# Performance work log

Measured on AMD Instinct MI355X. Metric: run time of the kernel, lower is better.

The kernel has to match this reference:

```python
import jax, jax.numpy as jnp
import numpy as np

N, C, E = 2048, 512, 8192
EPS = 1e-5
MASK_FILL = -10000.0


def layer_norm(h, g, b):
    m = jnp.mean(h, axis=-1, keepdims=True)
    v = jnp.mean(jnp.square(h - m), axis=-1, keepdims=True)
    return (h - m) * jax.lax.rsqrt(v + EPS) * g + b


def setup_inputs() -> dict:
    key = jax.random.key(0)
    ks = jax.random.split(key, 20)
    s = 1.0 / np.sqrt(C)
    inp = {
        "x": jax.random.normal(ks[0], (N, C), jnp.float32),
        "edge_index": jax.random.randint(ks[1], (2, E), 0, N, jnp.int64),
        "edge_attr": jax.random.normal(ks[2], (E, C), jnp.float32),
        "edge_masks": jax.random.randint(ks[3], (E, E), 0, 2, jnp.int32).astype(bool),
        # GraphConv.nn: Linear(C, C)
        "W_nn": jax.random.normal(ks[4], (C, C), jnp.float32) * s,
        "b_nn": jax.random.normal(ks[5], (C,), jnp.float32) * s,
        # att_nn: Linear(3C, C) -> Tanh -> Linear(C, 1, bias=False) -> LeakyReLU(0.2)
        "W_att1": jax.random.normal(ks[6], (C, 3 * C), jnp.float32) * (1.0 / np.sqrt(3 * C)),
        "b_att1": jax.random.normal(ks[7], (C,), jnp.float32) * s,
        "w_att2": jax.random.normal(ks[8], (C,), jnp.float32) * s,
        # root weight [C, C] and bias [C]
        "root": jax.random.normal(ks[9], (C, C), jnp.float32) * s,
        "bias": jax.random.normal(ks[10], (C,), jnp.float32) * s,
        # graph_block: LayerNorms + Linear(C, C)
        "gamma1": jnp.ones((C,), jnp.float32),
        "beta1": jnp.zeros((C,), jnp.float32),
        "gamma2": jnp.ones((C,), jnp.float32),
        "beta2": jnp.zeros((C,), jnp.float32),
        "W_lin": jax.random.normal(ks[11], (C, C), jnp.float32) * s,
        "b_lin": jax.random.normal(ks[12], (C,), jnp.float32) * s,
    }
    return inp


def reference(x, edge_index, edge_attr, edge_masks, W_nn, b_nn, W_att1, b_att1,
              w_att2, root, bias, gamma1, beta1, gamma2, beta2, W_lin, b_lin):
    src = edge_index[0]  # x_j (source)
    dst = edge_index[1]  # x_i (target), also aggregation index

    # shared linear on gathered endpoints and edge attrs  [E, C]
    h_i = x[dst] @ W_nn.T + b_nn
    h_j = x[src] @ W_nn.T + b_nn
    h_e = edge_attr @ W_nn.T + b_nn

    # attention MLP (dropout in eval mode = identity)
    cat = jnp.concatenate([h_i, h_j, h_e], axis=1)          # [E, 3C]
    hid = jnp.tanh(cat @ W_att1.T + b_att1)                  # [E, C]
    s = hid @ w_att2                                         # [E]
    s = jax.nn.leaky_relu(s, 0.2)

    # row-wise masked softmax of the broadcast score vector; keep only diagonal
    logits = jnp.where(edge_masks, s[None, :], MASK_FILL)    # [E, E]
    lse = jax.scipy.special.logsumexp(logits, axis=1)        # [E]
    diag_logit = jnp.where(jnp.diagonal(edge_masks), s, MASK_FILL)
    att_diag = jnp.exp(diag_logit - lse)                     # [E]

    msg = h_j * att_diag[:, None]                            # [E, C]
    aggr = jax.ops.segment_sum(msg, dst, num_segments=N)     # [N, C]

    out = aggr + x @ root + bias                             # update()

    # graph_block wrapper
    x1 = layer_norm(out, gamma1, beta1)
    x2 = layer_norm(x1 + (x1 @ W_lin.T + b_lin), gamma2, beta2)
    return x2
```

## Files before the change

### kernel.cpp

```cpp
#include <hip/hip_runtime.h>
#include <hip/hip_bf16.h>
#include <stdint.h>
#include <stddef.h>

#define NN 2048
#define CD 512
#define EE 8192

typedef unsigned short u16;
typedef __attribute__((ext_vector_type(8))) short short8;
typedef __attribute__((ext_vector_type(4))) float floatx4;

__device__ inline u16 f2bf(float f) {
    uint32_t u = __float_as_uint(f);
    u += 0x7FFFu + ((u >> 16) & 1u);
    return (u16)(u >> 16);
}
__device__ inline float bf2f(u16 h) { return __uint_as_float(((uint32_t)h) << 16); }

__global__ __launch_bounds__(256) void prep_kernel(
    const float* __restrict__ x, const float* __restrict__ ea,
    const float* __restrict__ Wnn, const float* __restrict__ Wlin,
    const float* __restrict__ root, const float* __restrict__ Watt1,
    u16* __restrict__ xb, u16* __restrict__ eb, u16* __restrict__ Wnnb,
    u16* __restrict__ Wlinb, u16* __restrict__ rootTb, u16* __restrict__ Wpackb)
{
    size_t idx = (size_t)blockIdx.x * 256 + threadIdx.x;
    if (idx < 1048576) { xb[idx] = f2bf(x[idx]); return; }
    idx -= 1048576;
    if (idx < 4194304) { eb[idx] = f2bf(ea[idx]); return; }
    idx -= 4194304;
    if (idx < 262144) { Wnnb[idx] = f2bf(Wnn[idx]); return; }
    idx -= 262144;
    if (idx < 262144) { Wlinb[idx] = f2bf(Wlin[idx]); return; }
    idx -= 262144;
    if (idx < 262144) {
        int c = (int)(idx >> 9), k = (int)(idx & 511);
        rootTb[idx] = f2bf(root[(size_t)k * 512 + c]); return;
    }
    idx -= 262144;
    {
        int cp = (int)(idx >> 9), k = (int)(idx & 511);
        int s = cp >> 9, c = cp & 511;
        Wpackb[idx] = f2bf(Watt1[(size_t)c * 1536 + s * 512 + k]);
    }
}

template<int BM, int BN, bool OUT_BF16, bool BIAS>
__global__ __launch_bounds__(256) void gemm_bt(
    const u16* __restrict__ A, const u16* __restrict__ B,
    void* __restrict__ Cout, const float* __restrict__ bias, int Nc)
{
    constexpr int K = 512, BK = 32;
    __shared__ __align__(16) u16 As[BM * BK];
    __shared__ __align__(16) u16 Bs[BN * BK];
    const int tid = threadIdx.x;
    const int bm = blockIdx.x, bn = blockIdx.y;
    const int wave = tid >> 6, lane = tid & 63;
    const int wm = wave >> 1, wn = wave & 1;
    constexpr int WM = BM / 2, WN = BN / 2;
    constexpr int FM = WM / 16, FN = WN / 16;
    const int lrow = lane & 15, lk = lane >> 4;
    floatx4 acc[FM][FN] = {};
    constexpr int ALOADS = (BM * BK) / (256 * 8);
    constexpr int BLOADS = (BN * BK) / (256 * 8);

    for (int k0 = 0; k0 < K; k0 += BK) {
        __syncthreads();
#pragma unroll
        for (int c = 0; c < ALOADS; ++c) {
            int e = c * 2048 + tid * 8;
            int row = e >> 5, col = e & 31;
            __builtin_amdgcn_global_load_lds(
                (const __attribute__((address_space(1))) void*)(A + (size_t)(bm * BM + row) * K + k0 + col),
                (__attribute__((address_space(3))) void*)(&As[e]), 16, 0, 0);
        }
#pragma unroll
        for (int c = 0; c < BLOADS; ++c) {
            int e = c * 2048 + tid * 8;
            int row = e >> 5, col = e & 31;
            __builtin_amdgcn_global_load_lds(
                (const __attribute__((address_space(1))) void*)(B + (size_t)(bn * BN + row) * K + k0 + col),
                (__attribute__((address_space(3))) void*)(&Bs[e]), 16, 0, 0);
        }
        __syncthreads();

        short8 af[FM], bfr[FN];
#pragma unroll
        for (int i = 0; i < FM; ++i)
            af[i] = *(const short8*)(&As[(wm * WM + i * 16 + lrow) * BK + lk * 8]);
#pragma unroll
        for (int j = 0; j < FN; ++j)
            bfr[j] = *(const short8*)(&Bs[(wn * WN + j * 16 + lrow) * BK + lk * 8]);
#pragma unroll
        for (int i = 0; i < FM; ++i)
#pragma unroll
            for (int j = 0; j < FN; ++j)
                acc[i][j] = __builtin_amdgcn_mfma_f32_16x16x32_bf16(af[i], bfr[j], acc[i][j], 0, 0, 0);
    }

#pragma unroll
    for (int i = 0; i < FM; ++i) {
#pragma unroll
        for (int j = 0; j < FN; ++j) {
            const int col = bn * BN + wn * WN + j * 16 + lrow;
            const float bv = BIAS ? bias[col] : 0.0f;
#pragma unroll
            for (int r = 0; r < 4; ++r) {
                const int row = bm * BM + wm * WM + i * 16 + lk * 4 + r;
                const float v = acc[i][j][r] + bv;
                if (OUT_BF16) ((u16*)Cout)[(size_t)row * Nc + col] = f2bf(v);
                else          ((float*)Cout)[(size_t)row * Nc + col] = v;
            }
        }
    }
}

__global__ __launch_bounds__(256) void edge_score(
    const float* __restrict__ G12, const float* __restrict__ G3,
    const int* __restrict__ ei, const float* __restrict__ batt1,
    const float* __restrict__ watt2, float* __restrict__ sOut)
{
    const int e = blockIdx.x;
    const int src = ei[e];
    const int dst = ei[EE + e];
    const int tid = threadIdx.x;
    const float* g1 = G12 + (size_t)dst * 1024;
    const float* g2 = G12 + (size_t)src * 1024 + 512;
    const float* g3 = G3 + (size_t)e * 512;
    float partial = 0.0f;
#pragma unroll
    for (int c = tid; c < 512; c += 256) {
        float v = tanhf(g1[c] + g2[c] + g3[c] + batt1[c]);
        partial += v * watt2[c];
    }
    for (int o = 32; o; o >>= 1) partial += __shfl_down(partial, o);
    __shared__ float red[4];
    if ((tid & 63) == 0) red[tid >> 6] = partial;
    __syncthreads();
    if (tid == 0) {
        float sv = red[0] + red[1] + red[2] + red[3];
        sOut[e] = (sv >= 0.0f) ? sv : 0.2f * sv;
    }
}

__global__ __launch_bounds__(1024) void softmax_prep(
    const float* __restrict__ s, float* __restrict__ p)
{
    const int tid = threadIdx.x;
    float m = -3.0e38f;
    for (int j = tid; j < EE; j += 1024) m = fmaxf(m, s[j]);
    for (int o = 32; o; o >>= 1) m = fmaxf(m, __shfl_down(m, o));
    __shared__ float red[16];
    if ((tid & 63) == 0) red[tid >> 6] = m;
    __syncthreads();
    float M = red[0];
#pragma unroll
    for (int k = 1; k < 16; ++k) M = fmaxf(M, red[k]);
    for (int j = tid; j < EE; j += 1024) p[j] = __expf(s[j] - M);
}

__global__ __launch_bounds__(256) void lse_att(
    const unsigned char* __restrict__ mask, const float* __restrict__ p,
    float* __restrict__ att)
{
    const int i = blockIdx.x;
    const int tid = threadIdx.x;
    const unsigned char* row = mask + (size_t)i * EE;
    float sum = 0.0f;
#pragma unroll
    for (int c = 0; c < 2; ++c) {
        const int base = c * 4096 + tid * 16;
        uint4 mw = *(const uint4*)(row + base);
        uint32_t w[4] = { mw.x, mw.y, mw.z, mw.w };
#pragma unroll
        for (int q = 0; q < 4; ++q) {
            float4 pv = *(const float4*)(p + base + q * 4);
            uint32_t b = w[q];
            sum += pv.x * (float)(b & 1u);
            sum += pv.y * (float)((b >> 8) & 1u);
            sum += pv.z * (float)((b >> 16) & 1u);
            sum += pv.w * (float)((b >> 24) & 1u);
        }
    }
    for (int o = 32; o; o >>= 1) sum += __shfl_down(sum, o);
    __shared__ float red[4];
    if ((tid & 63) == 0) red[tid >> 6] = sum;
    __syncthreads();
    if (tid == 0) {
        float total = red[0] + red[1] + red[2] + red[3];
        unsigned char diag = mask[(size_t)i * EE + i];
        float a;
        if (total > 0.0f) a = diag ? (p[i] / total) : 0.0f;
        else              a = 1.0f / (float)EE;
        att[i] = a;
    }
}

__global__ __launch_bounds__(256) void aggr_kernel(
    const u16* __restrict__ Hb, const int* __restrict__ ei,
    const float* __restrict__ att, float* __restrict__ OUT1)
{
    const int e = blockIdx.x;
    const float a = att[e];
    if (a == 0.0f) return;
    const int src = ei[e];
    const int dst = ei[EE + e];
    const u16* h = Hb + (size_t)src * 512;
    float* o = OUT1 + (size_t)dst * 512;
    for (int c = threadIdx.x; c < 512; c += 256)
        atomicAdd(o + c, a * bf2f(h[c]));
}

template<bool RESID, bool WRITE_BF16>
__global__ __launch_bounds__(256) void ln_kernel(
    const float* __restrict__ in, const float* __restrict__ resid,
    const float* __restrict__ gamma, const float* __restrict__ beta,
    float* __restrict__ outF, u16* __restrict__ outB)
{
    const int n = blockIdx.x, tid = threadIdx.x;
    const size_t rowoff = (size_t)n * 512;
    float2 v = *(const float2*)(in + rowoff + tid * 2);
    float a0 = v.x, a1 = v.y;
    if (RESID) {
        float2 r = *(const float2*)(resid + rowoff + tid * 2);
        a0 += r.x; a1 += r.y;
    }
    float sum = a0 + a1, sq = a0 * a0 + a1 * a1;
    for (int o = 32; o; o >>= 1) {
        sum += __shfl_down(sum, o);
        sq  += __shfl_down(sq, o);
    }
    __shared__ float rs_[4], rq_[4];
    if ((tid & 63) == 0) { rs_[tid >> 6] = sum; rq_[tid >> 6] = sq; }
    __syncthreads();
    sum = rs_[0] + rs_[1] + rs_[2] + rs_[3];
    sq  = rq_[0] + rq_[1] + rq_[2] + rq_[3];
    const float mean = sum * (1.0f / 512.0f);
    const float var  = sq * (1.0f / 512.0f) - mean * mean;
    const float rstd = rsqrtf(var + 1e-5f);
    const int c0 = tid * 2;
    const float y0 = (a0 - mean) * rstd * gamma[c0]     + beta[c0];
    const float y1 = (a1 - mean) * rstd * gamma[c0 + 1] + beta[c0 + 1];
    *(float2*)(outF + rowoff + c0) = make_float2(y0, y1);
    if (WRITE_BF16) { outB[rowoff + c0] = f2bf(y0); outB[rowoff + c0 + 1] = f2bf(y1); }
}

extern "C" void kernel_launch(void* const* d_in, const int* in_sizes, int n_in,
                              void* d_out, int out_size, void* d_ws, size_t ws_size,
                              hipStream_t stream)
{
    const float* x     = (const float*)d_in[0];
    const int*   ei    = (const int*)d_in[1];
    const float* ea    = (const float*)d_in[2];
    const unsigned char* mask = (const unsigned char*)d_in[3];
    const float* Wnn   = (const float*)d_in[4];
    const float* bnn   = (const float*)d_in[5];
    const float* Watt1 = (const float*)d_in[6];
    const float* batt1 = (const float*)d_in[7];
    const float* watt2 = (const float*)d_in[8];
    const float* root  = (const float*)d_in[9];
    const float* bias  = (const float*)d_in[10];
    const float* gam1  = (const float*)d_in[11];
    const float* bet1  = (const float*)d_in[12];
    const float* gam2  = (const float*)d_in[13];
    const float* bet2  = (const float*)d_in[14];
    const float* Wlin  = (const float*)d_in[15];
    const float* blin  = (const float*)d_in[16];
    float* out = (float*)d_out;

    char* w = (char*)d_ws;
    auto take = [&](size_t bytes) -> char* {
        char* pp = w;
        w += (bytes + 255) & ~(size_t)255;
        return pp;
    };
    u16*   xb     = (u16*)take((size_t)NN * CD * 2);
    u16*   eb     = (u16*)take((size_t)EE * CD * 2);
    u16*   Wnnb   = (u16*)take((size_t)CD * CD * 2);
    u16*   Wlinb  = (u16*)take((size_t)CD * CD * 2);
    u16*   rootTb = (u16*)take((size_t)CD * CD * 2);
    u16*   Wpb    = (u16*)take((size_t)3 * CD * CD * 2);
    u16*   Hb     = (u16*)take((size_t)NN * CD * 2);
    u16*   HEb    = (u16*)take((size_t)EE * CD * 2);
    float* G12    = (float*)take((size_t)NN * 1024 * 4);
    float* G3     = (float*)take((size_t)EE * CD * 4);
    float* OUT1   = (float*)take((size_t)NN * CD * 4);
    float* sbuf   = (float*)take((size_t)EE * 4);
    float* pbuf   = (float*)take((size_t)EE * 4);
    float* attb   = (float*)take((size_t)EE * 4);
    float* x1     = (float*)take((size_t)NN * CD * 4);
    u16*   x1b    = (u16*)take((size_t)NN * CD * 2);
    float* Tbuf   = (float*)take((size_t)NN * CD * 4);

    prep_kernel<<<26624, 256, 0, stream>>>(x, ea, Wnn, Wlin, root, Watt1,
                                           xb, eb, Wnnb, Wlinb, rootTb, Wpb);
    gemm_bt<64, 128, true, true><<<dim3(32, 4), 256, 0, stream>>>(xb, Wnnb, Hb, bnn, 512);
    gemm_bt<128, 128, true, true><<<dim3(64, 4), 256, 0, stream>>>(eb, Wnnb, HEb, bnn, 512);
    gemm_bt<64, 128, false, false><<<dim3(32, 8), 256, 0, stream>>>(Hb, Wpb, G12, nullptr, 1024);
    gemm_bt<128, 128, false, false><<<dim3(64, 4), 256, 0, stream>>>(HEb, Wpb + (size_t)1024 * 512, G3, nullptr, 512);
    gemm_bt<64, 128, false, true><<<dim3(32, 4), 256, 0, stream>>>(xb, rootTb, OUT1, bias, 512);
    edge_score<<<EE, 256, 0, stream>>>(G12, G3, ei, batt1, watt2, sbuf);
    softmax_prep<<<1, 1024, 0, stream>>>(sbuf, pbuf);
    lse_att<<<EE, 256, 0, stream>>>(mask, pbuf, attb);
    aggr_kernel<<<EE, 256, 0, stream>>>(Hb, ei, attb, OUT1);
    ln_kernel<false, true><<<NN, 256, 0, stream>>>(OUT1, nullptr, gam1, bet1, x1, x1b);
    gemm_bt<64, 128, false, true><<<dim3(32, 4), 256, 0, stream>>>(x1b, Wlinb, Tbuf, blin, 512);
    ln_kernel<true, false><<<NN, 256, 0, stream>>>(Tbuf, x1, gam2, bet2, out, nullptr);
}
```

Baseline: 465.1 us.

## Precompose attention weights with Wnn and fuse edge GEMM with tanh score reduction

Folds W_nn into the attention weights by precomputing Watt1·Wnn products and a combined bias vector, so the node and edge paths each need one GEMM. The x-side GEMMs (h, root, G12) run as one concatenated-B node GEMM. The edge GEMM now applies tanh and dot with w_att2 in its epilogue and accumulates scores atomically, removing the HEb and G3 intermediates and the separate edge_score pass. Also vectorizes prep conversion, processes four mask rows per block in lse_att, and vectorizes aggr loads. This changes bf16 rounding order, since products are quantized after composition, and adds atomics plus a memset.

```diff
diff --git a/kernel.cpp b/kernel.cpp
--- a/kernel.cpp
+++ b/kernel.cpp
@@ -1,5 +1,4 @@
 #include <hip/hip_runtime.h>
-#include <hip/hip_bf16.h>
 #include <stdint.h>
 #include <stddef.h>
 
@@ -22,49 +21,79 @@
     const float* __restrict__ x, const float* __restrict__ ea,
     const float* __restrict__ Wnn, const float* __restrict__ Wlin,
     const float* __restrict__ root, const float* __restrict__ Watt1,
-    u16* __restrict__ xb, u16* __restrict__ eb, u16* __restrict__ Wnnb,
-    u16* __restrict__ Wlinb, u16* __restrict__ rootTb, u16* __restrict__ Wpackb)
-{
-    size_t idx = (size_t)blockIdx.x * 256 + threadIdx.x;
-    if (idx < 1048576) { xb[idx] = f2bf(x[idx]); return; }
-    idx -= 1048576;
-    if (idx < 4194304) { eb[idx] = f2bf(ea[idx]); return; }
-    idx -= 4194304;
-    if (idx < 262144) { Wnnb[idx] = f2bf(Wnn[idx]); return; }
-    idx -= 262144;
-    if (idx < 262144) { Wlinb[idx] = f2bf(Wlin[idx]); return; }
-    idx -= 262144;
-    if (idx < 262144) {
-        int c = (int)(idx >> 9), k = (int)(idx & 511);
-        rootTb[idx] = f2bf(root[(size_t)k * 512 + c]); return;
-    }
-    idx -= 262144;
+    u16* __restrict__ xb, u16* __restrict__ eb, u16* __restrict__ Bcat,
+    u16* __restrict__ WnnTb, u16* __restrict__ Wlinb, u16* __restrict__ Wpackb)
+{
+    size_t i4 = ((size_t)blockIdx.x * 256 + threadIdx.x) * 4;
+    auto cvt4 = [](const float* src, u16* dst, size_t idx) {
+        float4 v = *(const float4*)(src + idx);
+        ushort4 o; o.x = f2bf(v.x); o.y = f2bf(v.y); o.z = f2bf(v.z); o.w = f2bf(v.w);
+        *(ushort4*)(dst + idx) = o;
+    };
+    if (i4 < 1048576) { cvt4(x, xb, i4); return; }
+    i4 -= 1048576;
+    if (i4 < 4194304) { cvt4(ea, eb, i4); return; }
+    i4 -= 4194304;
+    if (i4 < 262144) { cvt4(Wnn, Bcat, i4); return; }
+    i4 -= 262144;
+    if (i4 < 262144) {
+        int c = (int)(i4 >> 9), k = (int)(i4 & 511);
+        ushort4 o;
+        o.x = f2bf(root[(size_t)(k + 0) * 512 + c]);
+        o.y = f2bf(root[(size_t)(k + 1) * 512 + c]);
+        o.z = f2bf(root[(size_t)(k + 2) * 512 + c]);
+        o.w = f2bf(root[(size_t)(k + 3) * 512 + c]);
+        *(ushort4*)(Bcat + 262144 + i4) = o; return;
+    }
+    i4 -= 262144;
+    if (i4 < 262144) {
+        int k = (int)(i4 >> 9), t = (int)(i4 & 511);
+        ushort4 o;
+        o.x = f2bf(Wnn[(size_t)(t + 0) * 512 + k]);
+        o.y = f2bf(Wnn[(size_t)(t + 1) * 512 + k]);
+        o.z = f2bf(Wnn[(size_t)(t + 2) * 512 + k]);
+        o.w = f2bf(Wnn[(size_t)(t + 3) * 512 + k]);
+        *(ushort4*)(WnnTb + i4) = o; return;
+    }
+    i4 -= 262144;
+    if (i4 < 262144) { cvt4(Wlin, Wlinb, i4); return; }
+    i4 -= 262144;
     {
-        int cp = (int)(idx >> 9), k = (int)(idx & 511);
-        int s = cp >> 9, c = cp & 511;
-        Wpackb[idx] = f2bf(Watt1[(size_t)c * 1536 + s * 512 + k]);
-    }
-}
-
-template<int BM, int BN, bool OUT_BF16, bool BIAS>
-__global__ __launch_bounds__(256) void gemm_bt(
-    const u16* __restrict__ A, const u16* __restrict__ B,
-    void* __restrict__ Cout, const float* __restrict__ bias, int Nc)
-{
-    constexpr int K = 512, BK = 32;
-    __shared__ __align__(16) u16 As[BM * BK];
-    __shared__ __align__(16) u16 Bs[BN * BK];
-    const int tid = threadIdx.x;
-    const int bm = blockIdx.x, bn = blockIdx.y;
+        int cp = (int)(i4 >> 9), t = (int)(i4 & 511);
+        const float* sp = Watt1 + (size_t)(cp & 511) * 1536 + (cp >> 9) * 512 + t;
+        float4 v = *(const float4*)sp;
+        ushort4 o; o.x = f2bf(v.x); o.y = f2bf(v.y); o.z = f2bf(v.z); o.w = f2bf(v.w);
+        *(ushort4*)(Wpackb + i4) = o;
+    }
+}
+
+__global__ __launch_bounds__(256) void bbvec_kernel(
+    const float* __restrict__ Watt1, const float* __restrict__ bnn,
+    const float* __restrict__ batt1, float* __restrict__ bb)
+{
+    const int c = blockIdx.x, tid = threadIdx.x;
+    const float* row = Watt1 + (size_t)c * 1536;
+    float partial = 0.0f;
+#pragma unroll
+    for (int t = tid; t < 1536; t += 256) partial += row[t] * bnn[t & 511];
+    for (int o = 32; o; o >>= 1) partial += __shfl_down(partial, o);
+    __shared__ float red[4];
+    if ((tid & 63) == 0) red[tid >> 6] = partial;
+    __syncthreads();
+    if (tid == 0) bb[c] = batt1[c] + red[0] + red[1] + red[2] + red[3];
+}
+
+template<int BM, int BN>
+__device__ inline void gemm_core(const u16* __restrict__ A, const u16* __restrict__ B,
+                                 int bm, int bn, int tid, u16* As, u16* Bs,
+                                 floatx4 (&acc)[BM / 32][BN / 32])
+{
+    constexpr int K = 512, BK = 32, WM = BM / 2, WN = BN / 2, FM = WM / 16, FN = WN / 16;
     const int wave = tid >> 6, lane = tid & 63;
     const int wm = wave >> 1, wn = wave & 1;
-    constexpr int WM = BM / 2, WN = BN / 2;
-    constexpr int FM = WM / 16, FN = WN / 16;
     const int lrow = lane & 15, lk = lane >> 4;
-    floatx4 acc[FM][FN] = {};
     constexpr int ALOADS = (BM * BK) / (256 * 8);
     constexpr int BLOADS = (BN * BK) / (256 * 8);
-
     for (int k0 = 0; k0 < K; k0 += BK) {
         __syncthreads();
 #pragma unroll
@@ -84,7 +113,6 @@
                 (__attribute__((address_space(3))) void*)(&Bs[e]), 16, 0, 0);
         }
         __syncthreads();
-
         short8 af[FM], bfr[FN];
 #pragma unroll
         for (int i = 0; i < FM; ++i)
@@ -98,9 +126,23 @@
             for (int j = 0; j < FN; ++j)
                 acc[i][j] = __builtin_amdgcn_mfma_f32_16x16x32_bf16(af[i], bfr[j], acc[i][j], 0, 0, 0);
     }
-
-#pragma unroll
-    for (int i = 0; i < FM; ++i) {
+}
+
+template<int BM, int BN, bool OUT_BF16, bool BIAS>
+__global__ __launch_bounds__(256) void gemm_bt(
+    const u16* __restrict__ A, const u16* __restrict__ B,
+    void* __restrict__ Cout, const float* __restrict__ bias, int Nc)
+{
+    __shared__ __align__(16) u16 As[BM * 32];
+    __shared__ __align__(16) u16 Bs[BN * 32];
+    constexpr int WM = BM / 2, WN = BN / 2, FM = WM / 16, FN = WN / 16;
+    floatx4 acc[FM][FN] = {};
+    const int tid = threadIdx.x, bm = blockIdx.x, bn = blockIdx.y;
+    gemm_core<BM, BN>(A, B, bm, bn, tid, As, Bs, acc);
+    const int wave = tid >> 6, lane = tid & 63, wm = wave >> 1, wn = wave & 1;
+    const int lrow = lane & 15, lk = lane >> 4;
+#pragma unroll
+    for (int i = 0; i < FM; ++i)
 #pragma unroll
         for (int j = 0; j < FN; ++j) {
             const int col = bn * BN + wn * WN + j * 16 + lrow;
@@ -113,43 +155,89 @@
                 else          ((float*)Cout)[(size_t)row * Nc + col] = v;
             }
         }
-    }
-}
-
-__global__ __launch_bounds__(256) void edge_score(
-    const float* __restrict__ G12, const float* __restrict__ G3,
-    const int* __restrict__ ei, const float* __restrict__ batt1,
-    const float* __restrict__ watt2, float* __restrict__ sOut)
-{
-    const int e = blockIdx.x;
-    const int src = ei[e];
-    const int dst = ei[EE + e];
+}
+
+__global__ __launch_bounds__(256) void node_gemm(
+    const u16* __restrict__ A, const u16* __restrict__ B,
+    const float* __restrict__ bnn, const float* __restrict__ bias,
+    u16* __restrict__ Hb, float* __restrict__ OUT1, float* __restrict__ G12)
+{
+    __shared__ __align__(16) u16 As[128 * 32];
+    __shared__ __align__(16) u16 Bs[128 * 32];
+    floatx4 acc[4][4] = {};
+    const int tid = threadIdx.x, bm = blockIdx.x, bn = blockIdx.y;
+    gemm_core<128, 128>(A, B, bm, bn, tid, As, Bs, acc);
+    const int wave = tid >> 6, lane = tid & 63, wm = wave >> 1, wn = wave & 1;
+    const int lrow = lane & 15, lk = lane >> 4;
+#pragma unroll
+    for (int i = 0; i < 4; ++i)
+#pragma unroll
+        for (int j = 0; j < 4; ++j) {
+            const int colg = bn * 128 + wn * 64 + j * 16 + lrow;
+#pragma unroll
+            for (int r = 0; r < 4; ++r) {
+                const int row = bm * 128 + wm * 64 + i * 16 + lk * 4 + r;
+                const float v = acc[i][j][r];
+                if (bn < 4) {
+                    Hb[(size_t)row * 512 + colg] = f2bf(v + bnn[colg]);
+                } else if (bn < 8) {
+                    const int c = colg - 512;
+                    OUT1[(size_t)row * 512 + c] = v + bias[c];
+                } else {
+                    G12[(size_t)row * 1024 + (colg - 1024)] = v;
+                }
+            }
+        }
+}
+
+__global__ __launch_bounds__(256) void edge_gemm_score(
+    const u16* __restrict__ A, const u16* __restrict__ B,
+    const float* __restrict__ G12, const int* __restrict__ ei,
+    const float* __restrict__ bb, const float* __restrict__ w2,
+    float* __restrict__ sraw)
+{
+    __shared__ __align__(16) u16 As[128 * 32];
+    __shared__ __align__(16) u16 Bs[128 * 32];
+    floatx4 acc[4][4] = {};
+    const int tid = threadIdx.x, bm = blockIdx.x, bn = blockIdx.y;
+    gemm_core<128, 128>(A, B, bm, bn, tid, As, Bs, acc);
+    const int wave = tid >> 6, lane = tid & 63, wm = wave >> 1, wn = wave & 1;
+    const int lrow = lane & 15, lk = lane >> 4;
+#pragma unroll
+    for (int i = 0; i < 4; ++i) {
+#pragma unroll
+        for (int r = 0; r < 4; ++r) {
+            const int e = bm * 128 + wm * 64 + i * 16 + lk * 4 + r;
+            const int sn = ei[e], dn = ei[EE + e];
+            float sp = 0.0f;
+#pragma unroll
+            for (int j = 0; j < 4; ++j) {
+                const int col = bn * 128 + wn * 64 + j * 16 + lrow;
+                const float v = acc[i][j][r]
+                              + G12[(size_t)dn * 1024 + col]
+                              + G12[(size_t)sn * 1024 + 512 + col]
+                              + bb[col];
+                sp += tanhf(v) * w2[col];
+            }
+#pragma unroll
+            for (int m = 1; m < 16; m <<= 1) sp += __shfl_xor(sp, m);
+            if (lrow == 0) atomicAdd(sraw + e, sp);
+        }
+    }
+}
+
+__global__ __launch_bounds__(1024) void softmax_prep(
+    const float* __restrict__ sraw, float* __restrict__ p)
+{
     const int tid = threadIdx.x;
-    const float* g1 = G12 + (size_t)dst * 1024;
-    const float* g2 = G12 + (size_t)src * 1024 + 512;
-    const float* g3 = G3 + (size_t)e * 512;
-    float partial = 0.0f;
-#pragma unroll
-    for (int c = tid; c < 512; c += 256) {
-        float v = tanhf(g1[c] + g2[c] + g3[c] + batt1[c]);
-        partial += v * watt2[c];
-    }
-    for (int o = 32; o; o >>= 1) partial += __shfl_down(partial, o);
-    __shared__ float red[4];
-    if ((tid & 63) == 0) red[tid >> 6] = partial;
-    __syncthreads();
-    if (tid == 0) {
-        float sv = red[0] + red[1] + red[2] + red[3];
-        sOut[e] = (sv >= 0.0f) ? sv : 0.2f * sv;
-    }
-}
-
-__global__ __launch_bounds__(1024) void softmax_prep(
-    const float* __restrict__ s, float* __restrict__ p)
-{
-    const int tid = threadIdx.x;
+    float sv[8];
     float m = -3.0e38f;
-    for (int j = tid; j < EE; j += 1024) m = fmaxf(m, s[j]);
+#pragma unroll
+    for (int k = 0; k < 8; ++k) {
+        float v = sraw[k * 1024 + tid];
+        v = (v >= 0.0f) ? v : 0.2f * v;
+        sv[k] = v; m = fmaxf(m, v);
+    }
     for (int o = 32; o; o >>= 1) m = fmaxf(m, __shfl_down(m, o));
     __shared__ float red[16];
     if ((tid & 63) == 0) red[tid >> 6] = m;
@@ -157,39 +245,51 @@
     float M = red[0];
 #pragma unroll
     for (int k = 1; k < 16; ++k) M = fmaxf(M, red[k]);
-    for (int j = tid; j < EE; j += 1024) p[j] = __expf(s[j] - M);
+#pragma unroll
+    for (int k = 0; k < 8; ++k) p[k * 1024 + tid] = __expf(sv[k] - M);
 }
 
 __global__ __launch_bounds__(256) void lse_att(
     const unsigned char* __restrict__ mask, const float* __restrict__ p,
     float* __restrict__ att)
 {
-    const int i = blockIdx.x;
-    const int tid = threadIdx.x;
-    const unsigned char* row = mask + (size_t)i * EE;
-    float sum = 0.0f;
+    const int i0 = blockIdx.x * 4, tid = threadIdx.x;
+    float sums[4] = {0.0f, 0.0f, 0.0f, 0.0f};
 #pragma unroll
     for (int c = 0; c < 2; ++c) {
         const int base = c * 4096 + tid * 16;
-        uint4 mw = *(const uint4*)(row + base);
-        uint32_t w[4] = { mw.x, mw.y, mw.z, mw.w };
-#pragma unroll
-        for (int q = 0; q < 4; ++q) {
-            float4 pv = *(const float4*)(p + base + q * 4);
-            uint32_t b = w[q];
-            sum += pv.x * (float)(b & 1u);
-            sum += pv.y * (float)((b >> 8) & 1u);
-            sum += pv.z * (float)((b >> 16) & 1u);
-            sum += pv.w * (float)((b >> 24) & 1u);
-        }
-    }
-    for (int o = 32; o; o >>= 1) sum += __shfl_down(sum, o);
-    __shared__ float red[4];
-    if ((tid & 63) == 0) red[tid >> 6] = sum;
+        float pv[16];
+#pragma unroll
+        for (int q = 0; q < 4; ++q)
+            *(float4*)(pv + q * 4) = *(const float4*)(p + base + q * 4);
+#pragma unroll
+        for (int rr = 0; rr < 4; ++rr) {
+            uint4 mw = *(const uint4*)(mask + (size_t)(i0 + rr) * EE + base);
+            uint32_t w[4] = { mw.x, mw.y, mw.z, mw.w };
+            float s = 0.0f;
+#pragma unroll
+            for (int q = 0; q < 4; ++q) {
+                s += pv[q * 4 + 0] * (float)((w[q]      ) & 1u);
+                s += pv[q * 4 + 1] * (float)((w[q] >>  8) & 1u);
+                s += pv[q * 4 + 2] * (float)((w[q] >> 16) & 1u);
+                s += pv[q * 4 + 3] * (float)((w[q] >> 24) & 1u);
+            }
+            sums[rr] += s;
+        }
+    }
+#pragma unroll
+    for (int rr = 0; rr < 4; ++rr)
+        for (int o = 32; o; o >>= 1) sums[rr] += __shfl_down(sums[rr], o);
+    __shared__ float red[4][4];
+    if ((tid & 63) == 0) {
+#pragma unroll
+        for (int rr = 0; rr < 4; ++rr) red[rr][tid >> 6] = sums[rr];
+    }
     __syncthreads();
-    if (tid == 0) {
-        float total = red[0] + red[1] + red[2] + red[3];
-        unsigned char diag = mask[(size_t)i * EE + i];
+    if (tid < 4) {
+        const int i = i0 + tid;
+        const float total = red[tid][0] + red[tid][1] + red[tid][2] + red[tid][3];
+        const unsigned char diag = mask[(size_t)i * EE + i];
         float a;
         if (total > 0.0f) a = diag ? (p[i] / total) : 0.0f;
         else              a = 1.0f / (float)EE;
@@ -204,12 +304,13 @@
     const int e = blockIdx.x;
     const float a = att[e];
     if (a == 0.0f) return;
-    const int src = ei[e];
-    const int dst = ei[EE + e];
-    const u16* h = Hb + (size_t)src * 512;
-    float* o = OUT1 + (size_t)dst * 512;
-    for (int c = threadIdx.x; c < 512; c += 256)
-        atomicAdd(o + c, a * bf2f(h[c]));
+    const int sn = ei[e], dn = ei[EE + e];
+    const u16* h = Hb + (size_t)sn * 512;
+    float* o = OUT1 + (size_t)dn * 512;
+    const int c = threadIdx.x * 2;
+    const uint32_t hv = *(const uint32_t*)(h + c);
+    atomicAdd(o + c,     a * bf2f((u16)(hv & 0xffffu)));
+    atomicAdd(o + c + 1, a * bf2f((u16)(hv >> 16)));
 }
 
 template<bool RESID, bool WRITE_BF16>
@@ -227,10 +328,7 @@
         a0 += r.x; a1 += r.y;
     }
     float sum = a0 + a1, sq = a0 * a0 + a1 * a1;
-    for (int o = 32; o; o >>= 1) {
-        sum += __shfl_down(sum, o);
-        sq  += __shfl_down(sq, o);
-    }
+    for (int o = 32; o; o >>= 1) { sum += __shfl_down(sum, o); sq += __shfl_down(sq, o); }
     __shared__ float rs_[4], rq_[4];
     if ((tid & 63) == 0) { rs_[tid >> 6] = sum; rq_[tid >> 6] = sq; }
     __syncthreads();
@@ -271,38 +369,36 @@
 
     char* w = (char*)d_ws;
     auto take = [&](size_t bytes) -> char* {
-        char* pp = w;
-        w += (bytes + 255) & ~(size_t)255;
-        return pp;
+        char* pp = w; w += (bytes + 255) & ~(size_t)255; return pp;
     };
     u16*   xb     = (u16*)take((size_t)NN * CD * 2);
     u16*   eb     = (u16*)take((size_t)EE * CD * 2);
-    u16*   Wnnb   = (u16*)take((size_t)CD * CD * 2);
+    u16*   Wpackb = (u16*)take((size_t)1536 * CD * 2);
+    u16*   WnnTb  = (u16*)take((size_t)CD * CD * 2);
     u16*   Wlinb  = (u16*)take((size_t)CD * CD * 2);
-    u16*   rootTb = (u16*)take((size_t)CD * CD * 2);
-    u16*   Wpb    = (u16*)take((size_t)3 * CD * CD * 2);
+    u16*   Bcat   = (u16*)take((size_t)2560 * CD * 2);
     u16*   Hb     = (u16*)take((size_t)NN * CD * 2);
-    u16*   HEb    = (u16*)take((size_t)EE * CD * 2);
     float* G12    = (float*)take((size_t)NN * 1024 * 4);
-    float* G3     = (float*)take((size_t)EE * CD * 4);
     float* OUT1   = (float*)take((size_t)NN * CD * 4);
-    float* sbuf   = (float*)take((size_t)EE * 4);
+    float* sraw   = (float*)take((size_t)EE * 4);
     float* pbuf   = (float*)take((size_t)EE * 4);
     float* attb   = (float*)take((size_t)EE * 4);
+    float* bb     = (float*)take((size_t)CD * 4);
     float* x1     = (float*)take((size_t)NN * CD * 4);
     u16*   x1b    = (u16*)take((size_t)NN * CD * 2);
     float* Tbuf   = (float*)take((size_t)NN * CD * 4);
 
-    prep_kernel<<<26624, 256, 0, stream>>>(x, ea, Wnn, Wlin, root, Watt1,
-                                           xb, eb, Wnnb, Wlinb, rootTb, Wpb);
-    gemm_bt<64, 128, true, true><<<dim3(32, 4), 256, 0, stream>>>(xb, Wnnb, Hb, bnn, 512);
-    gemm_bt<128, 128, true, true><<<dim3(64, 4), 256, 0, stream>>>(eb, Wnnb, HEb, bnn, 512);
-    gemm_bt<64, 128, false, false><<<dim3(32, 8), 256, 0, stream>>>(Hb, Wpb, G12, nullptr, 1024);
-    gemm_bt<128, 128, false, false><<<dim3(64, 4), 256, 0, stream>>>(HEb, Wpb + (size_t)1024 * 512, G3, nullptr, 512);
-    gemm_bt<64, 128, false, true><<<dim3(32, 4), 256, 0, stream>>>(xb, rootTb, OUT1, bias, 512);
-    edge_score<<<EE, 256, 0, stream>>>(G12, G3, ei, batt1, watt2, sbuf);
-    softmax_prep<<<1, 1024, 0, stream>>>(sbuf, pbuf);
-    lse_att<<<EE, 256, 0, stream>>>(mask, pbuf, attb);
+    hipMemsetAsync(sraw, 0, (size_t)EE * 4, stream);
+    prep_kernel<<<6912, 256, 0, stream>>>(x, ea, Wnn, Wlin, root, Watt1,
+                                          xb, eb, Bcat, WnnTb, Wlinb, Wpackb);
+    bbvec_kernel<<<512, 256, 0, stream>>>(Watt1, bnn, batt1, bb);
+    gemm_bt<64, 128, true, false><<<dim3(24, 4), 256, 0, stream>>>(
+        Wpackb, WnnTb, Bcat + (size_t)1024 * 512, nullptr, 512);
+    node_gemm<<<dim3(16, 16), 256, 0, stream>>>(xb, Bcat, bnn, bias, Hb, OUT1, G12);
+    edge_gemm_score<<<dim3(64, 4), 256, 0, stream>>>(
+        eb, Bcat + (size_t)2048 * 512, G12, ei, bb, watt2, sraw);
+    softmax_prep<<<1, 1024, 0, stream>>>(sraw, pbuf);
+    lse_att<<<2048, 256, 0, stream>>>(mask, pbuf, attb);
     aggr_kernel<<<EE, 256, 0, stream>>>(Hb, ei, attb, OUT1);
     ln_kernel<false, true><<<NN, 256, 0, stream>>>(OUT1, nullptr, gam1, bet1, x1, x1b);
     gemm_bt<64, 128, false, true><<<dim3(32, 4), 256, 0, stream>>>(x1b, Wlinb, Tbuf, blin, 512);
```

Result: no change. 457.9 us (-1.6%).
